# Kernel optimization log

Measured on AMD Instinct MI355X. Metric: run time of the kernel, lower is better.

The kernel has to match this reference:

```python
import jax, jax.numpy as jnp
import numpy as np

V = 1_000_000   # num_embeddings
D = 64          # embedding_dim
B = 16_384      # number of bags (batch)
L = 50          # history length per bag


def setup_inputs() -> dict:
    key = jax.random.key(0)
    k_w, k_i = jax.random.split(key)
    weight = jax.random.normal(k_w, (V, D), dtype=jnp.float32) * 0.01
    indices = jax.random.randint(k_i, (B * L,), 0, V, dtype=jnp.int64)
    # bag start offsets (uniform bags of length L, starting at 0, sorted)
    offsets = (jnp.arange(B, dtype=jnp.int64) * L)
    return {"indices": indices, "offsets": offsets, "weight": weight}


def reference(indices, offsets, weight):
    """embedding_bag(indices, weight, offsets, mode='mean').

    indices: [T] int flat ids into weight rows
    offsets: [B] int bag start positions into indices (sorted, offsets[0]==0)
    weight:  [V, D] float embedding table
    returns: [B, D] per-bag mean of gathered embeddings
    """
    T = indices.shape[0]
    num_bags = offsets.shape[0]
    # bag id for each flat index position
    seg = jnp.searchsorted(offsets, jnp.arange(T), side="right") - 1  # [T]
    gathered = weight[indices]                                        # [T, D]
    sums = jax.ops.segment_sum(gathered, seg, num_segments=num_bags)  # [B, D]
    counts = jax.ops.segment_sum(
        jnp.ones((T,), dtype=weight.dtype), seg, num_segments=num_bags
    )                                                                 # [B]
    return sums / jnp.maximum(counts, 1.0)[:, None]
```

## Files before the change

kernel.cpp:

```cpp
#include <hip/hip_runtime.h>


constexpr int kBagsPerBlock = 16;
constexpr int kMaxFast = 64;

__global__ __launch_bounds__(256) void FreqAwareEmbedding_kernel(
    const int* __restrict__ indices,
    const int* __restrict__ offsets,
    const float4* __restrict__ weight4,
    float4* __restrict__ out4,
    int B, int T)
{
    __shared__ int sidx[kBagsPerBlock][kMaxFast + 1];

    const int tid = threadIdx.x;
    const int grp = tid >> 4;
    const int col = tid & 15;
    const int bag = blockIdx.x * kBagsPerBlock + grp;

    int start = 0, count = 0;
    if (bag < B) {
        start = offsets[bag];
        const int end = (bag + 1 < B) ? offsets[bag + 1] : T;
        count = end - start;
    }

    const bool fast = (count <= kMaxFast);
    if (fast) {
        for (int j = col; j < count; j += 16)
            sidx[grp][j] = indices[start + j];
    }
    __syncthreads();

    float4 acc = make_float4(0.f, 0.f, 0.f, 0.f);

    if (fast) {
        const int* sp = sidx[grp];
        int j = 0;
        for (; j + 10 <= count; j += 10) {
            int id[10];
            #pragma unroll
            for (int u = 0; u < 10; ++u) id[u] = sp[j + u];
            #pragma unroll
            for (int u = 0; u < 10; ++u) {
                const float4 v = weight4[(size_t)id[u] * 16 + col];
                acc.x += v.x; acc.y += v.y; acc.z += v.z; acc.w += v.w;
            }
        }
        for (; j < count; ++j) {
            const float4 v = weight4[(size_t)sp[j] * 16 + col];
            acc.x += v.x; acc.y += v.y; acc.z += v.z; acc.w += v.w;
        }
    } else if (count > 0) {
        for (int j = 0; j < count; ++j) {
            const float4 v = weight4[(size_t)indices[start + j] * 16 + col];
            acc.x += v.x; acc.y += v.y; acc.z += v.z; acc.w += v.w;
        }
    }

    if (bag < B) {
        const float inv = 1.0f / (float)((count > 0) ? count : 1);
        acc.x *= inv; acc.y *= inv; acc.z *= inv; acc.w *= inv;
        out4[(size_t)bag * 16 + col] = acc;
    }
}

extern "C" void kernel_launch(void* const* d_in, const int* in_sizes, int n_in,
                              void* d_out, int out_size, void* d_ws, size_t ws_size,
                              hipStream_t stream) {
    const int*   indices = (const int*)d_in[0];
    const int*   offsets = (const int*)d_in[1];
    const float* weight  = (const float*)d_in[2];

    const int T = in_sizes[0];
    const int B = in_sizes[1];

    const int grid = (B + kBagsPerBlock - 1) / kBagsPerBlock;

    FreqAwareEmbedding_kernel<<<grid, 256, 0, stream>>>(
        indices, offsets, (const float4*)weight, (float4*)d_out, B, T);
}
```

Baseline: 324.9 us.

## Slice embedding table by row range and sort gathers into cache-sized windows

Replaces the per-bag gather kernel with a two-stage scheme. Each block owns one of 8 row slices of the table and a set of bags, and bucket-sorts its indices into 4096-row windows in shared memory. It walks the windows in lockstep with a block-wide barrier, while coalesced prefetch loads warm each window in cache, aiming for L2/MALL locality on random gathers. A second kernel sums the 8 per-slice partials and divides by count, which adds workspace traffic, atomics, many barriers and redundant index reads.

```diff
diff --git a/kernel.cpp b/kernel.cpp
--- a/kernel.cpp
+++ b/kernel.cpp
@@ -1,10 +1,174 @@
 #include <hip/hip_runtime.h>
 
+
+constexpr int kMaxBPG = 8;
+constexpr int kWinShift = 12;
+constexpr int kMaxWin = 32;
+constexpr int kGroupCap = 512;
+
+__global__ __launch_bounds__(256, 4) void ebag_gather_sliced(
+    const int* __restrict__ indices,
+    const int* __restrict__ offsets,
+    const float4* __restrict__ weight4,
+    float4* __restrict__ part4,
+    int B, int T, int V, int bpg)
+{
+    __shared__ int ssort[16][kGroupCap];
+    __shared__ int scnt[16][kMaxWin];
+    __shared__ int sboff[16][kMaxWin + 1];
+    __shared__ int scur[16][kMaxWin];
+
+    const int tid = threadIdx.x;
+    const int grp = tid >> 4;
+    const int col = tid & 15;
+    const int slice = blockIdx.x & 7;
+    const int lid   = blockIdx.x >> 3;
+
+    const int slice_rows = (V + 7) >> 3;
+    const int sbase = slice * slice_rows;
+    const int send  = (sbase + slice_rows < V) ? (sbase + slice_rows) : V;
+    const int nwin  = (slice_rows + (1 << kWinShift) - 1) >> kWinShift;
+
+    for (int w = col; w < kMaxWin; w += 16) scnt[grp][w] = 0;
+
+    const int gis = lid * 16 + grp;
+    int bstart[kMaxBPG], bcnt[kMaxBPG];
+    #pragma unroll
+    for (int q = 0; q < kMaxBPG; ++q) {
+        bstart[q] = 0; bcnt[q] = 0;
+        if (q < bpg) {
+            const int bag = gis * bpg + q;
+            if (bag < B) {
+                const int s = offsets[bag];
+                const int e = (bag + 1 < B) ? offsets[bag + 1] : T;
+                bstart[q] = s; bcnt[q] = e - s;
+            }
+        }
+    }
+    __syncthreads();
+
+    #pragma unroll
+    for (int q = 0; q < kMaxBPG; ++q) {
+        if (q < bpg && bcnt[q] <= 64) {
+            for (int j = col; j < bcnt[q]; j += 16) {
+                const int idx = indices[bstart[q] + j];
+                if (idx >= sbase && idx < send)
+                    atomicAdd(&scnt[grp][(idx - sbase) >> kWinShift], 1);
+            }
+        }
+    }
+    __syncthreads();
+
+    if (col == 0) {
+        int run = 0;
+        for (int w = 0; w < nwin; ++w) {
+            sboff[grp][w] = run;
+            scur[grp][w]  = run;
+            run += scnt[grp][w];
+        }
+        sboff[grp][nwin] = run;
+    }
+    __syncthreads();
+
+    #pragma unroll
+    for (int q = 0; q < kMaxBPG; ++q) {
+        if (q < bpg && bcnt[q] <= 64) {
+            for (int j = col; j < bcnt[q]; j += 16) {
+                const int idx = indices[bstart[q] + j];
+                if (idx >= sbase && idx < send) {
+                    const int w = (idx - sbase) >> kWinShift;
+                    const int pos = atomicAdd(&scur[grp][w], 1);
+                    ssort[grp][pos] = (q << 20) | idx;
+                }
+            }
+        }
+    }
+
+    float4 acc[kMaxBPG];
+    #pragma unroll
+    for (int q = 0; q < kMaxBPG; ++q) acc[q] = make_float4(0.f, 0.f, 0.f, 0.f);
+
+    if (slice == 0) {
+        #pragma unroll
+        for (int q = 0; q < kMaxBPG; ++q) {
+            if (q < bpg && bcnt[q] > 64) {
+                for (int j = 0; j < bcnt[q]; ++j) {
+                    const int idx = indices[bstart[q] + j];
+                    const float4 v = weight4[(size_t)idx * 16 + col];
+                    acc[q].x += v.x; acc[q].y += v.y;
+                    acc[q].z += v.z; acc[q].w += v.w;
+                }
+            }
+        }
+    }
+    __syncthreads();
+
+    const long long gmaxf4 = (long long)V * 16;
+    float pfsink = 0.f;
+    for (int w = 0; w < nwin; ++w) {
+        float4 p0 = make_float4(0.f, 0.f, 0.f, 0.f), p1 = p0;
+        {
+            const long long winf4 = ((long long)sbase + ((long long)w << kWinShift)) * 16;
+            const long long i0 = winf4 + (long long)lid * 512 + tid;
+            if (i0 < gmaxf4)        p0 = weight4[i0];
+            if (i0 + 256 < gmaxf4)  p1 = weight4[i0 + 256];
+        }
+        for (int e = sboff[grp][w]; e < sboff[grp][w + 1]; ++e) {
+            const int packed = ssort[grp][e];
+            const int q   = packed >> 20;
+            const int row = packed & ((1 << 20) - 1);
+            const float4 v = weight4[(size_t)row * 16 + col];
+            #pragma unroll
+            for (int qq = 0; qq < kMaxBPG; ++qq) {
+                if (qq == q) {
+                    acc[qq].x += v.x; acc[qq].y += v.y;
+                    acc[qq].z += v.z; acc[qq].w += v.w;
+                }
+            }
+        }
+        pfsink += p0.x + p0.w + p1.x + p1.w;
+        __syncthreads();
+    }
+    asm volatile("" :: "v"(pfsink));
+
+    #pragma unroll
+    for (int q = 0; q < kMaxBPG; ++q) {
+        if (q < bpg) {
+            const int bag = gis * bpg + q;
+            if (bag < B)
+                part4[((size_t)slice * B + bag) * 16 + col] = acc[q];
+        }
+    }
+}
+
+__global__ __launch_bounds__(256) void ebag_reduce(
+    const int* __restrict__ offsets,
+    const float4* __restrict__ part4,
+    float4* __restrict__ out4,
+    int B, int T)
+{
+    const int g = blockIdx.x * blockDim.x + threadIdx.x;
+    if (g >= B * 16) return;
+    const int bag = g >> 4;
+    const int col = g & 15;
+    float4 s = make_float4(0.f, 0.f, 0.f, 0.f);
+    #pragma unroll
+    for (int sl = 0; sl < 8; ++sl) {
+        const float4 v = part4[((size_t)sl * B + bag) * 16 + col];
+        s.x += v.x; s.y += v.y; s.z += v.z; s.w += v.w;
+    }
+    const int st = offsets[bag];
+    const int en = (bag + 1 < B) ? offsets[bag + 1] : T;
+    const int c  = en - st;
+    const float inv = 1.0f / (float)((c > 0) ? c : 1);
+    s.x *= inv; s.y *= inv; s.z *= inv; s.w *= inv;
+    out4[(size_t)bag * 16 + col] = s;
+}
 
 constexpr int kBagsPerBlock = 16;
 constexpr int kMaxFast = 64;
 
-__global__ __launch_bounds__(256) void FreqAwareEmbedding_kernel(
+__global__ __launch_bounds__(256) void ebag_fallback(
     const int* __restrict__ indices,
     const int* __restrict__ offsets,
     const float4* __restrict__ weight4,
@@ -12,7 +176,6 @@
     int B, int T)
 {
     __shared__ int sidx[kBagsPerBlock][kMaxFast + 1];
-
     const int tid = threadIdx.x;
     const int grp = tid >> 4;
     const int col = tid & 15;
@@ -24,7 +187,6 @@
         const int end = (bag + 1 < B) ? offsets[bag + 1] : T;
         count = end - start;
     }
-
     const bool fast = (count <= kMaxFast);
     if (fast) {
         for (int j = col; j < count; j += 16)
@@ -33,21 +195,9 @@
     __syncthreads();
 
     float4 acc = make_float4(0.f, 0.f, 0.f, 0.f);
-
     if (fast) {
         const int* sp = sidx[grp];
-        int j = 0;
-        for (; j + 10 <= count; j += 10) {
-            int id[10];
-            #pragma unroll
-            for (int u = 0; u < 10; ++u) id[u] = sp[j + u];
-            #pragma unroll
-            for (int u = 0; u < 10; ++u) {
-                const float4 v = weight4[(size_t)id[u] * 16 + col];
-                acc.x += v.x; acc.y += v.y; acc.z += v.z; acc.w += v.w;
-            }
-        }
-        for (; j < count; ++j) {
+        for (int j = 0; j < count; ++j) {
             const float4 v = weight4[(size_t)sp[j] * 16 + col];
             acc.x += v.x; acc.y += v.y; acc.z += v.z; acc.w += v.w;
         }
@@ -57,7 +207,6 @@
             acc.x += v.x; acc.y += v.y; acc.z += v.z; acc.w += v.w;
         }
     }
-
     if (bag < B) {
         const float inv = 1.0f / (float)((count > 0) ? count : 1);
         acc.x *= inv; acc.y *= inv; acc.z *= inv; acc.w *= inv;
@@ -74,9 +223,23 @@
 
     const int T = in_sizes[0];
     const int B = in_sizes[1];
-
-    const int grid = (B + kBagsPerBlock - 1) / kBagsPerBlock;
-
-    FreqAwareEmbedding_kernel<<<grid, 256, 0, stream>>>(
-        indices, offsets, (const float4*)weight, (float4*)d_out, B, T);
-}
+    const int V = in_sizes[2] / 64;
+    const int bpg = (B + 2047) / 2048;
+    const size_t ws_need = (size_t)8 * (size_t)B * 256;
+
+    const bool main_path =
+        (in_sizes[2] % 64 == 0) && V >= 1 && V <= (1 << 20) &&
+        bpg >= 1 && bpg <= kMaxBPG && ws_size >= ws_need && d_ws != nullptr;
+
+    if (main_path) {
+        ebag_gather_sliced<<<1024, 256, 0, stream>>>(
+            indices, offsets, (const float4*)weight, (float4*)d_ws, B, T, V, bpg);
+        const int rthreads = B * 16;
+        ebag_reduce<<<(rthreads + 255) / 256, 256, 0, stream>>>(
+            offsets, (const float4*)d_ws, (float4*)d_out, B, T);
+    } else {
+        const int grid = (B + kBagsPerBlock - 1) / kBagsPerBlock;
+        ebag_fallback<<<grid, 256, 0, stream>>>(
+            indices, offsets, (const float4*)weight, (float4*)d_out, B, T);
+    }
+}
```

Measured after the change: 423.1 us. 30.2% more time.
